# Kernel optimization log

Hardware: AMD Instinct MI355X
Metric: run time of the kernel (lower is better)

Reference implementation:

```python
import jax, jax.numpy as jnp
import numpy as np
from jax import lax

MD = 3            # max displacement -> 7x7 = 49 correlation channels
WARP_WEIGHT = 2.5 # level 4


def leaky(x):
    return jnp.where(x >= 0, x, 0.1 * x)


def conv2d(x, w, b, pad):
    y = lax.conv_general_dilated(x, w, (1, 1), [(pad, pad), (pad, pad)],
                                 dimension_numbers=('NCHW', 'OIHW', 'NCHW'))
    return y + b[None, :, None, None]


def upflow(flow, w):
    # torch ConvTranspose2d(2,2,k=4,s=2,p=1,groups=2,bias=False), weight [in=2, out/g=1, 4, 4]
    wf = w[:, :, ::-1, ::-1]  # spatial flip -> equivalent regular conv kernel (OIHW, O=2, I=1)
    return lax.conv_general_dilated(flow, wf, (1, 1), [(2, 2), (2, 2)],
                                    lhs_dilation=(2, 2),
                                    dimension_numbers=('NCHW', 'OIHW', 'NCHW'),
                                    feature_group_count=2)


def backwarp(feat, flow):
    # bilinear backward warp, zero padding outside image (pixel coords + flow)
    B, C, H, W = feat.shape
    gy = jnp.arange(H, dtype=feat.dtype)[None, :, None] + flow[:, 1]  # [B,H,W]
    gx = jnp.arange(W, dtype=feat.dtype)[None, None, :] + flow[:, 0]
    x0 = jnp.floor(gx); y0 = jnp.floor(gy)
    wx = gx - x0; wy = gy - y0
    x0i = x0.astype(jnp.int32); y0i = y0.astype(jnp.int32)
    fB = feat.transpose(0, 2, 3, 1)  # [B,H,W,C]
    bidx = jnp.arange(B)[:, None, None]

    def gather(yi, xi):
        yc = jnp.clip(yi, 0, H - 1); xc = jnp.clip(xi, 0, W - 1)
        v = fB[bidx, yc, xc]  # [B,H,W,C]
        valid = ((yi >= 0) & (yi < H) & (xi >= 0) & (xi < W)).astype(feat.dtype)
        return v * valid[..., None]

    out = (gather(y0i, x0i) * ((1 - wy) * (1 - wx))[..., None]
           + gather(y0i, x0i + 1) * ((1 - wy) * wx)[..., None]
           + gather(y0i + 1, x0i) * (wy * (1 - wx))[..., None]
           + gather(y0i + 1, x0i + 1) * (wy * wx)[..., None])
    return out.transpose(0, 3, 1, 2)


def correlation(f1, f2):
    # windowed cost volume: mean over channels of f1 * shifted f2, shifts in [-MD,MD]^2
    B, C, H, W = f1.shape
    f2p = jnp.pad(f2, ((0, 0), (0, 0), (MD, MD), (MD, MD)))
    outs = []
    for dy in range(-MD, MD + 1):
        for dx in range(-MD, MD + 1):
            sl = f2p[:, :, MD + dy:MD + dy + H, MD + dx:MD + dx + W]
            outs.append(jnp.mean(f1 * sl, axis=1))  # [B,H,W]
    return jnp.stack(outs, axis=1)  # [B,49,H,W]


def setup_inputs() -> dict:
    key = jax.random.key(0)
    ks = jax.random.split(key, 16)
    B, C, H, W = 4, 96, 192, 192
    inp = {
        'tensor1': jax.random.normal(ks[0], (B, 3, 1536, 1536), jnp.float32),
        'tensor2': jax.random.normal(ks[1], (B, 3, 1536, 1536), jnp.float32),
        'features_tensor1': jax.random.normal(ks[2], (B, C, H, W), jnp.float32),
        'features_tensor2': jax.random.normal(ks[3], (B, C, H, W), jnp.float32),
        'flow_tensor': jax.random.normal(ks[4], (B, 2, H // 2, W // 2), jnp.float32),
        'w_upflow': jax.random.normal(ks[5], (2, 1, 4, 4), jnp.float32) * 0.25,
        'w1': jax.random.normal(ks[6], (128, 49, 3, 3), jnp.float32) * 0.05,
        'b1': jnp.zeros((128,), jnp.float32),
        'w2': jax.random.normal(ks[7], (64, 128, 3, 3), jnp.float32) * 0.05,
        'b2': jnp.zeros((64,), jnp.float32),
        'w3': jax.random.normal(ks[8], (32, 64, 3, 3), jnp.float32) * 0.05,
        'b3': jnp.zeros((32,), jnp.float32),
        'w4': jax.random.normal(ks[9], (2, 32, 5, 5), jnp.float32) * 0.05,
        'b4': jnp.zeros((2,), jnp.float32),
    }
    return inp


def reference(tensor1, tensor2, features_tensor1, features_tensor2, flow_tensor,
              w_upflow, w1, b1, w2, b2, w3, b3, w4, b4):
    # level 4: moduleFeat is identity
    flow = upflow(flow_tensor, w_upflow)                       # [B,2,192,192]
    feat2 = backwarp(features_tensor2, flow * WARP_WEIGHT)
    corr = leaky(correlation(features_tensor1, feat2))          # [B,49,192,192]
    x = leaky(conv2d(corr, w1, b1, 1))
    x = leaky(conv2d(x, w2, b2, 1))
    x = leaky(conv2d(x, w3, b3, 1))
    x = conv2d(x, w4, b4, 2)                                    # kernel 5, pad 2 at level 4
    return flow + x
```

## Files before the change

kernel.cpp:

```cpp
#include <hip/hip_runtime.h>
#include <hip/hip_bf16.h>

#define HW 192
#define HWHW 36864
#define NB 4

typedef __attribute__((ext_vector_type(8))) short short8;
typedef __attribute__((ext_vector_type(4))) float floatx4;

__device__ __forceinline__ unsigned pack_bf2(float a, float b) {
    __hip_bfloat162 h = __float22bfloat162_rn(make_float2(a, b));
    return *(unsigned*)&h;
}
__device__ __forceinline__ float4 ld_bf16x4(const __hip_bfloat16* p) {
    uint2 u = *(const uint2*)p;
    __hip_bfloat162 a = *(__hip_bfloat162*)&u.x;
    __hip_bfloat162 b = *(__hip_bfloat162*)&u.y;
    float2 fa = __bfloat1622float2(a), fb = __bfloat1622float2(b);
    return make_float4(fa.x, fa.y, fb.x, fb.y);
}
__device__ __forceinline__ void st_bf16x4(__hip_bfloat16* p, float4 v) {
    uint2 u;
    u.x = pack_bf2(v.x, v.y);
    u.y = pack_bf2(v.z, v.w);
    *(uint2*)p = u;
}

__global__ void upflow_kernel(const float* __restrict__ fin,
                              const float* __restrict__ w,
                              float* __restrict__ fout) {
    int idx = blockIdx.x * blockDim.x + threadIdx.x;
    if (idx >= NB * 2 * HWHW) return;
    int x = idx % HW;
    int y = (idx / HW) % HW;
    int g = (idx / HWHW) % 2;
    int b = idx / (2 * HWHW);
    float acc = 0.f;
#pragma unroll
    for (int ky = 0; ky < 4; ++ky) {
        int py = y + ky - 2;
        if (py < 0 || py > 190 || (py & 1)) continue;
        int iy = py >> 1;
#pragma unroll
        for (int kx = 0; kx < 4; ++kx) {
            int px = x + kx - 2;
            if (px < 0 || px > 190 || (px & 1)) continue;
            int ix = px >> 1;
            acc += fin[((b * 2 + g) * 96 + iy) * 96 + ix] *
                   w[g * 16 + (3 - ky) * 4 + (3 - kx)];
        }
    }
    fout[idx] = acc;
}

__global__ void wprep_kernel(const float* __restrict__ w, __hip_bfloat16* __restrict__ out,
                             int CO, int CI, int CIP) {
    int idx = blockIdx.x * blockDim.x + threadIdx.x;
    int n = 9 * CO * CIP;
    if (idx >= n) return;
    int ci = idx % CIP;
    int co = (idx / CIP) % CO;
    int k9 = idx / (CIP * CO);
    float v = (ci < CI) ? w[(co * CI + ci) * 9 + k9] : 0.f;
    out[idx] = __float2bfloat16(v);
}

__global__ __launch_bounds__(256) void backwarp_kernel(const float* __restrict__ feat,
                                                       const float* __restrict__ flow,
                                                       __hip_bfloat16* __restrict__ out) {
    int p = blockIdx.x * blockDim.x + threadIdx.x;
    if (p >= NB * HWHW) return;
    int cg = blockIdx.y;
    int x = p % HW;
    int y = (p / HW) % HW;
    int b = p / HWHW;
    float fx = flow[((b * 2 + 0) * HW + y) * HW + x] * 2.5f;
    float fy = flow[((b * 2 + 1) * HW + y) * HW + x] * 2.5f;
    float gx = (float)x + fx, gy = (float)y + fy;
    float x0f = floorf(gx), y0f = floorf(gy);
    float wx = gx - x0f, wy = gy - y0f;
    int x0 = (int)x0f, y0 = (int)y0f;
    bool xv0 = (unsigned)x0 < (unsigned)HW;
    bool xv1 = (unsigned)(x0 + 1) < (unsigned)HW;
    bool yv0 = (unsigned)y0 < (unsigned)HW;
    bool yv1 = (unsigned)(y0 + 1) < (unsigned)HW;
    float w00 = (1.f - wy) * (1.f - wx) * ((yv0 && xv0) ? 1.f : 0.f);
    float w01 = (1.f - wy) * wx * ((yv0 && xv1) ? 1.f : 0.f);
    float w10 = wy * (1.f - wx) * ((yv1 && xv0) ? 1.f : 0.f);
    float w11 = wy * wx * ((yv1 && xv1) ? 1.f : 0.f);
    int xc0 = min(max(x0, 0), HW - 1), xc1 = min(max(x0 + 1, 0), HW - 1);
    int yc0 = min(max(y0, 0), HW - 1), yc1 = min(max(y0 + 1, 0), HW - 1);
    const float* fb = feat + (size_t)b * 96 * HWHW + (size_t)cg * 24 * HWHW;
    int i00 = yc0 * HW + xc0, i01 = yc0 * HW + xc1;
    int i10 = yc1 * HW + xc0, i11 = yc1 * HW + xc1;
    __hip_bfloat16* op = out + (size_t)p * 96 + cg * 24;
#pragma unroll
    for (int c = 0; c < 24; c += 8) {
        float r[8];
#pragma unroll
        for (int j = 0; j < 8; ++j) {
            const float* fc = fb + (size_t)(c + j) * HWHW;
            r[j] = w00 * fc[i00] + w01 * fc[i01] + w10 * fc[i10] + w11 * fc[i11];
        }
        uint4 u;
        u.x = pack_bf2(r[0], r[1]);
        u.y = pack_bf2(r[2], r[3]);
        u.z = pack_bf2(r[4], r[5]);
        u.w = pack_bf2(r[6], r[7]);
        *(uint4*)&op[c] = u;
    }
}

__global__ __launch_bounds__(256) void corr_kernel(const float* __restrict__ f1,
                                                   const __hip_bfloat16* __restrict__ f2,
                                                   __hip_bfloat16* __restrict__ out) {
    __shared__ float s1[16][16][4];
    __shared__ float s2[22][23][4];
    int t = threadIdx.x;
    int tx = t % 16, ty = t / 16;
    int x0 = blockIdx.x * 16, y0 = blockIdx.y * 16, b = blockIdx.z;
    float acc[49];
#pragma unroll
    for (int i = 0; i < 49; ++i) acc[i] = 0.f;

    for (int c0 = 0; c0 < 96; c0 += 4) {
        __syncthreads();
        {
            int gy = y0 + ty, gx = x0 + tx;
#pragma unroll
            for (int i = 0; i < 4; ++i)
                s1[ty][tx][i] = f1[((b * 96 + c0 + i) * HWHW) + gy * HW + gx];
        }
        for (int p = t; p < 22 * 22; p += 256) {
            int ry = p / 22, rx = p % 22;
            int gy = y0 + ry - 3, gx = x0 + rx - 3;
            bool v = ((unsigned)gy < (unsigned)HW) && ((unsigned)gx < (unsigned)HW);
            float4 vv = make_float4(0.f, 0.f, 0.f, 0.f);
            if (v) vv = ld_bf16x4(&f2[(size_t)((b * HW + gy) * HW + gx) * 96 + c0]);
            *(float4*)&s2[ry][rx][0] = vv;
        }
        __syncthreads();
        float4 v1 = *(const float4*)&s1[ty][tx][0];
#pragma unroll
        for (int dy = 0; dy < 7; ++dy) {
#pragma unroll
            for (int dx = 0; dx < 7; ++dx) {
                float4 v2 = *(const float4*)&s2[ty + dy][tx + dx][0];
                acc[dy * 7 + dx] += v1.x * v2.x + v1.y * v2.y + v1.z * v2.z + v1.w * v2.w;
            }
        }
    }
    int gy = y0 + ty, gx = x0 + tx;
    __hip_bfloat16* op = out + (size_t)((b * HW + gy) * HW + gx) * 64;
#pragma unroll
    for (int d0 = 0; d0 < 64; d0 += 4) {
        float vv[4];
#pragma unroll
        for (int j = 0; j < 4; ++j) {
            int d = d0 + j;
            float a = (d < 49) ? acc[d] * (1.0f / 96.0f) : 0.f;
            a = a >= 0.f ? a : 0.1f * a;
            vv[j] = a;
        }
        st_bf16x4(op + d0, make_float4(vv[0], vv[1], vv[2], vv[3]));
    }
}

template <int CIN, int COUT, int WAVES_CO, int WCO, int LEAKY>
__global__ __launch_bounds__(256) void convk(const __hip_bfloat16* __restrict__ in,
                                             const __hip_bfloat16* __restrict__ wg,
                                             const float* __restrict__ bias,
                                             __hip_bfloat16* __restrict__ out) {
    constexpr int WAVES_PX = 4 / WAVES_CO;
    constexpr int BR = WAVES_PX * 4;
    constexpr int CIS = 36;
    static_assert(WAVES_CO * WCO * 16 == COUT, "one co-block covers all COUT");
    __shared__ __hip_bfloat16 s_in[BR * 18 * CIS];
    __shared__ __hip_bfloat16 s_w[3 * COUT * CIS];

    const int t = threadIdx.x;
    const int lane = t & 63;
    const int wave = t >> 6;
    const int q = lane >> 4;
    const int l16 = lane & 15;
    const int wr = wave % WAVES_PX;
    const int wc = wave / WAVES_PX;
    const int x0 = blockIdx.x * 16;
    const int y0 = blockIdx.y * BR;
    const int b = blockIdx.z;

    floatx4 acc[4][WCO];
#pragma unroll
    for (int i = 0; i < 4; ++i)
#pragma unroll
        for (int j = 0; j < WCO; ++j) acc[i][j] = (floatx4){0.f, 0.f, 0.f, 0.f};

    for (int ci0 = 0; ci0 < CIN; ci0 += 32) {
#pragma unroll
        for (int ky = 0; ky < 3; ++ky) {
            __syncthreads();
            for (int ch = t; ch < BR * 18 * 4; ch += 256) {
                int c8 = (ch & 3) * 8;
                int px = ch >> 2;
                int s = px / 18, cc = px % 18;
                int gy = y0 + s + ky - 1, gx = x0 + cc - 1;
                uint4 u = make_uint4(0u, 0u, 0u, 0u);
                if ((unsigned)gy < (unsigned)HW && (unsigned)gx < (unsigned)HW)
                    u = *(const uint4*)&in[(size_t)((b * HW + gy) * HW + gx) * CIN + ci0 + c8];
                *(uint4*)&s_in[(s * 18 + cc) * CIS + c8] = u;
            }
            for (int ch = t; ch < 3 * COUT * 4; ch += 256) {
                int c8 = (ch & 3) * 8;
                int co = (ch >> 2) % COUT;
                int kx = ch / (COUT * 4);
                *(uint4*)&s_w[(kx * COUT + co) * CIS + c8] =
                    *(const uint4*)&wg[(size_t)((ky * 3 + kx) * COUT + co) * CIN + ci0 + c8];
            }
            __syncthreads();
#pragma unroll
            for (int kx = 0; kx < 3; ++kx) {
                short8 A[WCO], B[4];
#pragma unroll
                for (int ct = 0; ct < WCO; ++ct)
                    A[ct] = *(const short8*)&s_w[(kx * COUT + wc * WCO * 16 + ct * 16 + l16) * CIS + q * 8];
#pragma unroll
                for (int pt = 0; pt < 4; ++pt)
                    B[pt] = *(const short8*)&s_in[((wr * 4 + pt) * 18 + l16 + kx) * CIS + q * 8];
#pragma unroll
                for (int pt = 0; pt < 4; ++pt)
#pragma unroll
                    for (int ct = 0; ct < WCO; ++ct)
                        acc[pt][ct] = __builtin_amdgcn_mfma_f32_16x16x32_bf16(A[ct], B[pt], acc[pt][ct], 0, 0, 0);
            }
        }
    }
#pragma unroll
    for (int pt = 0; pt < 4; ++pt) {
        int y = y0 + wr * 4 + pt;
        int x = x0 + l16;
        size_t pixbase = (size_t)((b * HW + y) * HW + x) * COUT;
#pragma unroll
        for (int ct = 0; ct < WCO; ++ct) {
            int co4 = wc * WCO * 16 + ct * 16 + q * 4;
            float4 bv = *(const float4*)&bias[co4];
            float r[4];
#pragma unroll
            for (int reg = 0; reg < 4; ++reg) {
                float vv = acc[pt][ct][reg] + ((const float*)&bv)[reg];
                if (LEAKY) vv = vv >= 0.f ? vv : 0.1f * vv;
                r[reg] = vv;
            }
            uint2 u;
            u.x = pack_bf2(r[0], r[1]);
            u.y = pack_bf2(r[2], r[3]);
            *(uint2*)&out[pixbase + co4] = u;
        }
    }
}

__global__ __launch_bounds__(256) void conv4_kernel(const __hip_bfloat16* __restrict__ in,
                                                    const float* __restrict__ wg,
                                                    const float* __restrict__ bias,
                                                    const float* __restrict__ flow,
                                                    float* __restrict__ out) {
    __shared__ float s_in[20 * 20 * 36];
    __shared__ float s_w[2 * 25 * 32];
    int t = threadIdx.x;
    int tx = t % 16, ty = t / 16;
    int x0 = blockIdx.x * 16, y0 = blockIdx.y * 16, b = blockIdx.z;
    for (int ch = t; ch < 400 * 4; ch += 256) {
        int px = ch >> 2;
        int c8 = (ch & 3) * 8;
        int ry = px / 20, rx = px % 20;
        int gy = y0 + ry - 2, gx = x0 + rx - 2;
        float4 lo = make_float4(0.f, 0.f, 0.f, 0.f), hi = lo;
        if ((unsigned)gy < (unsigned)HW && (unsigned)gx < (unsigned)HW) {
            const __hip_bfloat16* p = &in[(size_t)((b * HW + gy) * HW + gx) * 32 + c8];
            lo = ld_bf16x4(p);
            hi = ld_bf16x4(p + 4);
        }
        *(float4*)&s_in[px * 36 + c8] = lo;
        *(float4*)&s_in[px * 36 + c8 + 4] = hi;
    }
    for (int p = t; p < 1600; p += 256) {
        int ci = p % 32;
        int k = (p / 32) % 25;
        int co = p / 800;
        s_w[(co * 25 + k) * 32 + ci] = wg[(co * 32 + ci) * 25 + k];
    }
    __syncthreads();
    float acc0 = 0.f, acc1 = 0.f;
#pragma unroll
    for (int ky = 0; ky < 5; ++ky) {
#pragma unroll
        for (int kx = 0; kx < 5; ++kx) {
            int k = ky * 5 + kx;
            int base = ((ty + ky) * 20 + tx + kx) * 36;
#pragma unroll
            for (int c4 = 0; c4 < 32; c4 += 4) {
                float4 v = *(const float4*)&s_in[base + c4];
                float4 w0 = *(const float4*)&s_w[(0 * 25 + k) * 32 + c4];
                float4 w1 = *(const float4*)&s_w[(1 * 25 + k) * 32 + c4];
                acc0 += v.x * w0.x + v.y * w0.y + v.z * w0.z + v.w * w0.w;
                acc1 += v.x * w1.x + v.y * w1.y + v.z * w1.z + v.w * w1.w;
            }
        }
    }
    int gy = y0 + ty, gx = x0 + tx;
    int o0 = ((b * 2 + 0) * HWHW) + gy * HW + gx;
    int o1 = ((b * 2 + 1) * HWHW) + gy * HW + gx;
    out[o0] = acc0 + bias[0] + flow[o0];
    out[o1] = acc1 + bias[1] + flow[o1];
}

extern "C" void kernel_launch(void* const* d_in, const int* in_sizes, int n_in,
                              void* d_out, int out_size, void* d_ws, size_t ws_size,
                              hipStream_t stream) {
    (void)in_sizes; (void)n_in; (void)out_size; (void)ws_size;
    const float* f1      = (const float*)d_in[2];
    const float* f2in    = (const float*)d_in[3];
    const float* flow_in = (const float*)d_in[4];
    const float* w_up    = (const float*)d_in[5];
    const float* w1      = (const float*)d_in[6];
    const float* b1      = (const float*)d_in[7];
    const float* w2      = (const float*)d_in[8];
    const float* b2      = (const float*)d_in[9];
    const float* w3      = (const float*)d_in[10];
    const float* b3      = (const float*)d_in[11];
    const float* w4      = (const float*)d_in[12];
    const float* b4      = (const float*)d_in[13];
    float* out = (float*)d_out;
    char* ws = (char*)d_ws;

    float* flow = (float*)ws;
    __hip_bfloat16* w1b = (__hip_bfloat16*)(ws + 1179648);
    __hip_bfloat16* w2b = (__hip_bfloat16*)(ws + 1327104);
    __hip_bfloat16* w3b = (__hip_bfloat16*)(ws + 1474560);
    __hip_bfloat16* R1  = (__hip_bfloat16*)(ws + 1511424);
    __hip_bfloat16* R2  = (__hip_bfloat16*)(ws + 39260160);
    __hip_bfloat16* R3  = (__hip_bfloat16*)(ws + 58134528);

    upflow_kernel<<<1152, 256, 0, stream>>>(flow_in, w_up, flow);
    wprep_kernel<<<288, 256, 0, stream>>>(w1, w1b, 128, 49, 64);
    wprep_kernel<<<288, 256, 0, stream>>>(w2, w2b, 64, 128, 128);
    wprep_kernel<<<72, 256, 0, stream>>>(w3, w3b, 32, 64, 64);
    backwarp_kernel<<<dim3(576, 4), 256, 0, stream>>>(f2in, flow, R1);
    corr_kernel<<<dim3(12, 12, NB), 256, 0, stream>>>(f1, R1, R2);
    convk<64, 128, 2, 4, 1><<<dim3(12, 24, NB), 256, 0, stream>>>(R2, w1b, b1, R1);
    convk<128, 64, 1, 4, 1><<<dim3(12, 12, NB), 256, 0, stream>>>(R1, w2b, b2, R2);
    convk<64, 32, 1, 2, 1><<<dim3(12, 12, NB), 256, 0, stream>>>(R2, w3b, b3, R3);
    conv4_kernel<<<dim3(12, 12, NB), 256, 0, stream>>>(R3, w4, b4, flow, out);
}
```

Baseline: 590.7 us.

## Compute correlation cost volume with bf16 MFMA using hi/lo split of f1

Replaces the scalar FP32 correlation kernel with one that casts the 7x7 windowed dot products as 16x16x32 bf16 MFMA tiles, computing a 16-pixel by 32-column product per displacement row and extracting the diagonal band. f1 is split into bf16 high and low parts so precision stays close to fp32 on that operand. Results are scattered through shared memory and written out with vectorised stores. It does redundant MFMA work, since only 7 of 32 columns per row are used, and it changes tile shape to 4 rows by 16 columns per block.

```diff
diff --git a/kernel.cpp b/kernel.cpp
--- a/kernel.cpp
+++ b/kernel.cpp
@@ -111,58 +111,100 @@
     }
 }
 
-__global__ __launch_bounds__(256) void corr_kernel(const float* __restrict__ f1,
-                                                   const __hip_bfloat16* __restrict__ f2,
-                                                   __hip_bfloat16* __restrict__ out) {
-    __shared__ float s1[16][16][4];
-    __shared__ float s2[22][23][4];
-    int t = threadIdx.x;
-    int tx = t % 16, ty = t / 16;
-    int x0 = blockIdx.x * 16, y0 = blockIdx.y * 16, b = blockIdx.z;
-    float acc[49];
-#pragma unroll
-    for (int i = 0; i < 49; ++i) acc[i] = 0.f;
-
-    for (int c0 = 0; c0 < 96; c0 += 4) {
+#define CIS2 40
+__global__ __launch_bounds__(256) void corr_mfma_kernel(const float* __restrict__ f1,
+                                                        const __hip_bfloat16* __restrict__ f2,
+                                                        __hip_bfloat16* __restrict__ out) {
+    __shared__ __hip_bfloat16 s_f1h[4 * 16 * CIS2];
+    __shared__ __hip_bfloat16 s_f1l[4 * 16 * CIS2];
+    __shared__ __hip_bfloat16 s_f2[10 * 22 * CIS2];
+    __shared__ float s_out[4][16][52];
+
+    const int t = threadIdx.x;
+    const int lane = t & 63;
+    const int wave = t >> 6;
+    const int q = lane >> 4;
+    const int l16 = lane & 15;
+    const int x0 = blockIdx.x * 16;
+    const int y0 = blockIdx.y * 4;
+    const int b = blockIdx.z;
+
+    floatx4 acc[7][2];
+#pragma unroll
+    for (int d = 0; d < 7; ++d)
+#pragma unroll
+        for (int nt = 0; nt < 2; ++nt) acc[d][nt] = (floatx4){0.f, 0.f, 0.f, 0.f};
+
+    for (int ci0 = 0; ci0 < 96; ci0 += 32) {
         __syncthreads();
-        {
-            int gy = y0 + ty, gx = x0 + tx;
-#pragma unroll
-            for (int i = 0; i < 4; ++i)
-                s1[ty][tx][i] = f1[((b * 96 + c0 + i) * HWHW) + gy * HW + gx];
-        }
-        for (int p = t; p < 22 * 22; p += 256) {
-            int ry = p / 22, rx = p % 22;
-            int gy = y0 + ry - 3, gx = x0 + rx - 3;
-            bool v = ((unsigned)gy < (unsigned)HW) && ((unsigned)gx < (unsigned)HW);
-            float4 vv = make_float4(0.f, 0.f, 0.f, 0.f);
-            if (v) vv = ld_bf16x4(&f2[(size_t)((b * HW + gy) * HW + gx) * 96 + c0]);
-            *(float4*)&s2[ry][rx][0] = vv;
+        for (int idx = t; idx < 1024; idx += 256) {
+            int px = idx & 15;
+            int cp = (idx >> 4) & 15;
+            int row = idx >> 8;
+            const float* p = f1 + (size_t)(b * 96 + ci0 + cp * 2) * HWHW + (y0 + row) * HW + (x0 + px);
+            float v0 = p[0], v1 = p[HWHW];
+            float h0 = __bfloat162float(__float2bfloat16(v0));
+            float h1 = __bfloat162float(__float2bfloat16(v1));
+            int o = (row * 16 + px) * CIS2 + cp * 2;
+            *(unsigned*)&s_f1h[o] = pack_bf2(v0, v1);
+            *(unsigned*)&s_f1l[o] = pack_bf2(v0 - h0, v1 - h1);
+        }
+        for (int idx = t; idx < 10 * 22 * 4; idx += 256) {
+            int c16 = idx & 3;
+            int c = (idx >> 2) % 22;
+            int rr = idx / 88;
+            int gy = y0 + rr - 3, gx = x0 + c - 3;
+            uint4 u = make_uint4(0u, 0u, 0u, 0u);
+            if ((unsigned)gy < (unsigned)HW && (unsigned)gx < (unsigned)HW)
+                u = *(const uint4*)&f2[(size_t)((b * HW + gy) * HW + gx) * 96 + ci0 + c16 * 8];
+            *(uint4*)&s_f2[(rr * 22 + c) * CIS2 + c16 * 8] = u;
         }
         __syncthreads();
-        float4 v1 = *(const float4*)&s1[ty][tx][0];
-#pragma unroll
-        for (int dy = 0; dy < 7; ++dy) {
-#pragma unroll
-            for (int dx = 0; dx < 7; ++dx) {
-                float4 v2 = *(const float4*)&s2[ty + dy][tx + dx][0];
-                acc[dy * 7 + dx] += v1.x * v2.x + v1.y * v2.y + v1.z * v2.z + v1.w * v2.w;
-            }
-        }
-    }
-    int gy = y0 + ty, gx = x0 + tx;
-    __hip_bfloat16* op = out + (size_t)((b * HW + gy) * HW + gx) * 64;
-#pragma unroll
-    for (int d0 = 0; d0 < 64; d0 += 4) {
-        float vv[4];
-#pragma unroll
-        for (int j = 0; j < 4; ++j) {
-            int d = d0 + j;
-            float a = (d < 49) ? acc[d] * (1.0f / 96.0f) : 0.f;
-            a = a >= 0.f ? a : 0.1f * a;
-            vv[j] = a;
-        }
-        st_bf16x4(op + d0, make_float4(vv[0], vv[1], vv[2], vv[3]));
+        short8 Ah = *(const short8*)&s_f1h[(wave * 16 + l16) * CIS2 + q * 8];
+        short8 Al = *(const short8*)&s_f1l[(wave * 16 + l16) * CIS2 + q * 8];
+#pragma unroll
+        for (int d = 0; d < 7; ++d) {
+#pragma unroll
+            for (int nt = 0; nt < 2; ++nt) {
+                int col = nt * 16 + l16;
+                col = col < 22 ? col : 21;
+                short8 B = *(const short8*)&s_f2[((wave + d) * 22 + col) * CIS2 + q * 8];
+                acc[d][nt] = __builtin_amdgcn_mfma_f32_16x16x32_bf16(Ah, B, acc[d][nt], 0, 0, 0);
+                acc[d][nt] = __builtin_amdgcn_mfma_f32_16x16x32_bf16(Al, B, acc[d][nt], 0, 0, 0);
+            }
+        }
+    }
+#pragma unroll
+    for (int d = 0; d < 7; ++d)
+#pragma unroll
+        for (int nt = 0; nt < 2; ++nt)
+#pragma unroll
+            for (int reg = 0; reg < 4; ++reg) {
+                int p1 = q * 4 + reg;
+                int dx = nt * 16 + l16 - p1;
+                if (dx >= 0 && dx < 7) s_out[wave][p1][d * 7 + dx] = acc[d][nt][reg];
+            }
+    __syncthreads();
+    {
+        int px = t >> 2;
+        int row = px >> 4, xl = px & 15;
+        int ch0 = (t & 3) * 16;
+        int gy = y0 + row, gx = x0 + xl;
+        float r[16];
+#pragma unroll
+        for (int j = 0; j < 16; ++j) {
+            int ch = ch0 + j;
+            float a = (ch < 49) ? s_out[row][xl][ch] * (1.0f / 96.0f) : 0.f;
+            r[j] = a >= 0.f ? a : 0.1f * a;
+        }
+        __hip_bfloat16* op = out + (size_t)((b * HW + gy) * HW + gx) * 64 + ch0;
+        uint4 u0, u1;
+        u0.x = pack_bf2(r[0], r[1]);  u0.y = pack_bf2(r[2], r[3]);
+        u0.z = pack_bf2(r[4], r[5]);  u0.w = pack_bf2(r[6], r[7]);
+        u1.x = pack_bf2(r[8], r[9]);  u1.y = pack_bf2(r[10], r[11]);
+        u1.z = pack_bf2(r[12], r[13]); u1.w = pack_bf2(r[14], r[15]);
+        *(uint4*)op = u0;
+        *(uint4*)(op + 8) = u1;
     }
 }
 
@@ -345,7 +387,7 @@
     wprep_kernel<<<288, 256, 0, stream>>>(w2, w2b, 64, 128, 128);
     wprep_kernel<<<72, 256, 0, stream>>>(w3, w3b, 32, 64, 64);
     backwarp_kernel<<<dim3(576, 4), 256, 0, stream>>>(f2in, flow, R1);
-    corr_kernel<<<dim3(12, 12, NB), 256, 0, stream>>>(f1, R1, R2);
+    corr_mfma_kernel<<<dim3(12, 48, NB), 256, 0, stream>>>(f1, R1, R2);
     convk<64, 128, 2, 4, 1><<<dim3(12, 24, NB), 256, 0, stream>>>(R2, w1b, b1, R1);
     convk<128, 64, 1, 4, 1><<<dim3(12, 12, NB), 256, 0, stream>>>(R1, w2b, b2, R2);
     convk<64, 32, 1, 2, 1><<<dim3(12, 12, NB), 256, 0, stream>>>(R2, w3b, b3, R3);
```

New measurement: 542.8 us. 1.09x faster.
